# Optimization experiments

Measured on AMD Instinct MI355X. Metric: run time of the kernel, lower is better.

## Reference

```python
import jax, jax.numpy as jnp
import numpy as np

GH, GW, B, H, OUT = 9, 9, 1024, 256, 1


def setup_inputs() -> dict:
    key = jax.random.key(0)
    ks = jax.random.split(key, 16)
    N = GH * GW
    s3 = 1.0 / np.sqrt(3 * H)
    sH = 1.0 / np.sqrt(H)
    return {
        "x": jax.random.normal(ks[0], (B, GH, GW), jnp.float32),
        "h_ext": jax.random.normal(ks[1], (B, H), jnp.float32),
        "c_ext": jax.random.normal(ks[2], (B, H), jnp.float32),
        "grid_h": jax.random.normal(ks[3], (GH, GW, B, H), jnp.float32),
        "grid_c": jax.random.normal(ks[4], (GH, GW, B, H), jnp.float32),
        "W_hp": jax.random.normal(ks[5], (N, H, 3 * H), jnp.float32) * s3,
        "b_hp": jax.random.normal(ks[6], (N, H), jnp.float32) * s3,
        "W_cp": jax.random.normal(ks[7], (N, H, 3 * H), jnp.float32) * s3,
        "b_cp": jax.random.normal(ks[8], (N, H), jnp.float32) * s3,
        "W_ih": jax.random.normal(ks[9], (N, 4 * H, 1), jnp.float32) * sH,
        "W_hh": jax.random.normal(ks[10], (N, 4 * H, H), jnp.float32) * sH,
        "b_ih": jax.random.normal(ks[11], (N, 4 * H), jnp.float32) * sH,
        "b_hh": jax.random.normal(ks[12], (N, 4 * H), jnp.float32) * sH,
        "W_out": jax.random.normal(ks[13], (OUT, H), jnp.float32) * sH,
        "b_out": jnp.zeros((OUT,), jnp.float32),
    }


def _lstm_cell(x_cell, h0, c0, W_ih_k, W_hh_k, b_ih_k, b_hh_k):
    # x_cell: [B,1], h0/c0: [B,H]; torch LSTMCell math
    gates = x_cell @ W_ih_k.T + b_ih_k + h0 @ W_hh_k.T + b_hh_k  # [B,4H]
    i, f, g, o = jnp.split(gates, 4, axis=1)
    i, f, o = jax.nn.sigmoid(i), jax.nn.sigmoid(f), jax.nn.sigmoid(o)
    g = jnp.tanh(g)
    c = f * c0 + i * g
    h = o * jnp.tanh(c)
    return h, c


def reference(x, h_ext, c_ext, grid_h, grid_c,
              W_hp, b_hp, W_cp, b_cp,
              W_ih, W_hh, b_ih, b_hh, W_out, b_out):
    zeros = jnp.zeros((B, H), x.dtype)
    # new states, updated in raster order; left/up neighbors read NEW states
    new_h = [[None] * GW for _ in range(GH)]
    new_c = [[None] * GW for _ in range(GH)]
    for i in range(GH):
        for j in range(GW):
            k = i * GW + j
            h_prev, c_prev = grid_h[i, j], grid_c[i, j]
            if i == 0 and j == 0:
                h_left, c_left = h_ext, c_ext
            elif j > 0:
                h_left, c_left = new_h[i][j - 1], new_c[i][j - 1]
            else:
                h_left, c_left = zeros, zeros
            if i > 0:
                h_up, c_up = new_h[i - 1][j], new_c[i - 1][j]
            else:
                h_up, c_up = zeros, zeros
            comb_h = jnp.concatenate([h_left, h_up, h_prev], axis=1)  # [B,3H]
            comb_c = jnp.concatenate([c_left, c_up, c_prev], axis=1)
            ph = comb_h @ W_hp[k].T + b_hp[k]
            pc = comb_c @ W_cp[k].T + b_cp[k]
            x_cell = x[:, i, j][:, None]  # [B,1]
            h_new, c_new = _lstm_cell(x_cell, ph, pc, W_ih[k], W_hh[k], b_ih[k], b_hh[k])
            new_h[i][j], new_c[i][j] = h_new, c_new
    final_h, final_c = new_h[-1][-1], new_c[-1][-1]
    # fc_out with fc_layers_out=[0]: Linear + ReLU, then sigmoid
    out = jax.nn.sigmoid(jax.nn.relu(final_h @ W_out.T + b_out))
    gh = jnp.stack([jnp.stack(r, 0) for r in new_h], 0)
    gc = jnp.stack([jnp.stack(r, 0) for r in new_c], 0)
    return out, final_h, final_c, gh, gc
```

## Files before the change

### kernel.cpp

```cpp
#include <hip/hip_runtime.h>
#include <math.h>

#define BATCH 1024
#define HID 256
#define W3 768
#define SLOT (BATCH * HID)

typedef __bf16 bf16_t;
typedef __bf16 bf16x8 __attribute__((ext_vector_type(8)));
typedef float f32x4 __attribute__((ext_vector_type(4)));

__device__ inline bf16x8 cvt8(const float4 a, const float4 b) {
    bf16x8 r;
    r[0] = (bf16_t)a.x; r[1] = (bf16_t)a.y; r[2] = (bf16_t)a.z; r[3] = (bf16_t)a.w;
    r[4] = (bf16_t)b.x; r[5] = (bf16_t)b.y; r[6] = (bf16_t)b.z; r[7] = (bf16_t)b.w;
    return r;
}

template<bool ATOMIC>
__device__ __forceinline__ void proj_core(
        const float* __restrict__ src, const float* __restrict__ W, int koff,
        const float* __restrict__ bias, float* __restrict__ out,
        bf16_t (*Asm)[40], bf16_t (*Bsm)[40]) {
    const int t = threadIdx.x;
    const int lane = t & 63, wid = t >> 6;
    const int wm = wid & 1, wn = wid >> 1;
    const int ln = lane & 15, lh = lane >> 4;
    const int b0 = blockIdx.x * 128, n0 = blockIdx.y * 128;
    const int sr = t >> 1, sq = (t & 1) * 16;
    const float* arow = src + (size_t)(b0 + sr) * HID + sq;
    const float* wrow = W + (size_t)(n0 + sr) * W3 + koff + sq;
    f32x4 acc[4][4] = {};
    for (int kb = 0; kb < 8; ++kb) {
        const float4 a0 = *(const float4*)(arow + kb * 32);
        const float4 a1 = *(const float4*)(arow + kb * 32 + 4);
        const float4 a2 = *(const float4*)(arow + kb * 32 + 8);
        const float4 a3 = *(const float4*)(arow + kb * 32 + 12);
        const float4 w0 = *(const float4*)(wrow + kb * 32);
        const float4 w1 = *(const float4*)(wrow + kb * 32 + 4);
        const float4 w2 = *(const float4*)(wrow + kb * 32 + 8);
        const float4 w3 = *(const float4*)(wrow + kb * 32 + 12);
        const bf16x8 av0 = cvt8(a0, a1), av1 = cvt8(a2, a3);
        const bf16x8 bv0 = cvt8(w0, w1), bv1 = cvt8(w2, w3);
        __syncthreads();
        *(bf16x8*)&Asm[sr][sq] = av0;
        *(bf16x8*)&Asm[sr][sq + 8] = av1;
        *(bf16x8*)&Bsm[sr][sq] = bv0;
        *(bf16x8*)&Bsm[sr][sq + 8] = bv1;
        __syncthreads();
        bf16x8 af[4], bfv[4];
        #pragma unroll
        for (int mf = 0; mf < 4; ++mf)
            af[mf] = *(const bf16x8*)&Asm[wm * 64 + mf * 16 + ln][lh * 8];
        #pragma unroll
        for (int nf = 0; nf < 4; ++nf)
            bfv[nf] = *(const bf16x8*)&Bsm[wn * 64 + nf * 16 + ln][lh * 8];
        #pragma unroll
        for (int mf = 0; mf < 4; ++mf)
            #pragma unroll
            for (int nf = 0; nf < 4; ++nf)
                acc[mf][nf] = __builtin_amdgcn_mfma_f32_16x16x32_bf16(
                    af[mf], bfv[nf], acc[mf][nf], 0, 0, 0);
    }
    #pragma unroll
    for (int nf = 0; nf < 4; ++nf) {
        const int n = n0 + wn * 64 + nf * 16 + ln;
        const float bn = ATOMIC ? 0.f : bias[n];
        #pragma unroll
        for (int mf = 0; mf < 4; ++mf)
            #pragma unroll
            for (int r = 0; r < 4; ++r) {
                const int b = b0 + wm * 64 + mf * 16 + lh * 4 + r;
                if (ATOMIC)
                    unsafeAtomicAdd(out + (size_t)b * HID + n, acc[mf][nf][r]);
                else
                    out[(size_t)b * HID + n] = acc[mf][nf][r] + bn;
            }
    }
}

__global__ __launch_bounds__(256) void prevproj_kernel(
        const float* __restrict__ gridh, const float* __restrict__ gridc,
        const float* __restrict__ Whp, const float* __restrict__ Wcp,
        const float* __restrict__ bhp, const float* __restrict__ bcp,
        float* __restrict__ pall) {
    __shared__ bf16_t As[128][40];
    __shared__ bf16_t Bs[128][40];
    const int z = blockIdx.z, k = z >> 1, hc = z & 1;
    const float* src = (hc ? gridc : gridh) + (size_t)k * SLOT;
    const float* W = (hc ? Wcp : Whp) + (size_t)k * HID * W3;
    const float* bias = (hc ? bcp : bhp) + (size_t)k * HID;
    proj_core<false>(src, W, 512, bias, pall + (size_t)z * SLOT, As, Bs);
}

struct SegDesc { const float* src; const float* W; const float* bias; float* out; int koff; };
struct SegArgs { SegDesc d[36]; };

__global__ __launch_bounds__(256) void projseg_kernel(SegArgs a) {
    __shared__ bf16_t As[128][40];
    __shared__ bf16_t Bs[128][40];
    const SegDesc d = a.d[blockIdx.z];
    if (d.bias) proj_core<false>(d.src, d.W, d.koff, d.bias, d.out, As, Bs);
    else        proj_core<true>(d.src, d.W, d.koff, nullptr, d.out, As, Bs);
}

struct CellDesc {
    const float* ph; const float* pc;
    const float* Whh; const float* Wih; const float* bih; const float* bhh;
    const float* xcol;
    float* gh; float* gc;
};
struct CellBatchArgs { CellDesc d[9]; };

__global__ __launch_bounds__(256) void cell_kernel(CellBatchArgs args) {
    const CellDesc cd = args.d[blockIdx.z];
    __shared__ bf16_t Psm[128][40];
    __shared__ bf16_t Wsm[128][40];
    const int t = threadIdx.x;
    const int lane = t & 63, wid = t >> 6;
    const int wm = wid & 1, wn = wid >> 1;
    const int ln = lane & 15, lh = lane >> 4;
    const int b0 = blockIdx.x * 128;
    const int u0 = blockIdx.y * 32;
    const int sr = t >> 1, sq = (t & 1) * 16;
    const float* prow = cd.ph + (size_t)(b0 + sr) * HID + sq;
    const int cg = sr >> 5, cdu = sr & 31;
    const float* wrow = cd.Whh + (size_t)(cg * HID + u0 + cdu) * HID + sq;

    f32x4 acc[4][4] = {};
    for (int kb = 0; kb < 8; ++kb) {
        const float4 p0 = *(const float4*)(prow + kb * 32);
        const float4 p1 = *(const float4*)(prow + kb * 32 + 4);
        const float4 p2 = *(const float4*)(prow + kb * 32 + 8);
        const float4 p3 = *(const float4*)(prow + kb * 32 + 12);
        const float4 w0 = *(const float4*)(wrow + kb * 32);
        const float4 w1 = *(const float4*)(wrow + kb * 32 + 4);
        const float4 w2 = *(const float4*)(wrow + kb * 32 + 8);
        const float4 w3 = *(const float4*)(wrow + kb * 32 + 12);
        const bf16x8 pv0 = cvt8(p0, p1), pv1 = cvt8(p2, p3);
        const bf16x8 wv0 = cvt8(w0, w1), wv1 = cvt8(w2, w3);
        __syncthreads();
        *(bf16x8*)&Psm[sr][sq] = pv0;
        *(bf16x8*)&Psm[sr][sq + 8] = pv1;
        *(bf16x8*)&Wsm[sr][sq] = wv0;
        *(bf16x8*)&Wsm[sr][sq + 8] = wv1;
        __syncthreads();
        bf16x8 af[4], bfr[4];
        #pragma unroll
        for (int mf = 0; mf < 4; ++mf)
            af[mf] = *(const bf16x8*)&Psm[wm * 64 + mf * 16 + ln][lh * 8];
        #pragma unroll
        for (int g = 0; g < 4; ++g)
            bfr[g] = *(const bf16x8*)&Wsm[g * 32 + wn * 16 + ln][lh * 8];
        #pragma unroll
        for (int mf = 0; mf < 4; ++mf)
            #pragma unroll
            for (int g = 0; g < 4; ++g)
                acc[mf][g] = __builtin_amdgcn_mfma_f32_16x16x32_bf16(
                    af[mf], bfr[g], acc[mf][g], 0, 0, 0);
    }

    const int u = u0 + wn * 16 + ln;
    float wih[4], bsum[4];
    #pragma unroll
    for (int g = 0; g < 4; ++g) {
        const int n = g * HID + u;
        wih[g] = cd.Wih[n];
        bsum[g] = cd.bih[n] + cd.bhh[n];
    }
    #pragma unroll
    for (int mf = 0; mf < 4; ++mf)
        #pragma unroll
        for (int r = 0; r < 4; ++r) {
            const int b = b0 + wm * 64 + mf * 16 + lh * 4 + r;
            const float xv = cd.xcol[(size_t)b * 81];
            const float gi = acc[mf][0][r] + xv * wih[0] + bsum[0];
            const float gf = acc[mf][1][r] + xv * wih[1] + bsum[1];
            const float gg = acc[mf][2][r] + xv * wih[2] + bsum[2];
            const float go = acc[mf][3][r] + xv * wih[3] + bsum[3];
            const float i_ = 1.f / (1.f + expf(-gi));
            const float f_ = 1.f / (1.f + expf(-gf));
            const float o_ = 1.f / (1.f + expf(-go));
            const float g_ = tanhf(gg);
            const float c0 = cd.pc[(size_t)b * HID + u];
            const float cn = f_ * c0 + i_ * g_;
            const float hn = o_ * tanhf(cn);
            cd.gh[(size_t)b * HID + u] = hn;
            cd.gc[(size_t)b * HID + u] = cn;
        }
}

__global__ __launch_bounds__(256) void final_kernel(
        const float* __restrict__ gh88, const float* __restrict__ gc88,
        const float* __restrict__ Wout, const float* __restrict__ bout,
        float* __restrict__ out, float* __restrict__ fh, float* __restrict__ fc) {
    const int tid = blockIdx.x * blockDim.x + threadIdx.x;
    const int nth = gridDim.x * blockDim.x;
    for (int idx = tid; idx < BATCH * HID; idx += nth) {
        fh[idx] = gh88[idx];
        fc[idx] = gc88[idx];
    }
    if (tid < BATCH) {
        float s = bout[0];
        for (int k = 0; k < HID; ++k) s += gh88[(size_t)tid * HID + k] * Wout[k];
        s = fmaxf(s, 0.f);
        out[tid] = 1.f / (1.f + expf(-s));
    }
}

extern "C" void kernel_launch(void* const* d_in, const int* in_sizes, int n_in,
                              void* d_out, int out_size, void* d_ws, size_t ws_size,
                              hipStream_t stream) {
    const float* x      = (const float*)d_in[0];
    const float* h_ext  = (const float*)d_in[1];
    const float* c_ext  = (const float*)d_in[2];
    const float* grid_h = (const float*)d_in[3];
    const float* grid_c = (const float*)d_in[4];
    const float* W_hp   = (const float*)d_in[5];
    const float* b_hp   = (const float*)d_in[6];
    const float* W_cp   = (const float*)d_in[7];
    const float* b_cp   = (const float*)d_in[8];
    const float* W_ih   = (const float*)d_in[9];
    const float* W_hh   = (const float*)d_in[10];
    const float* b_ih   = (const float*)d_in[11];
    const float* b_hh   = (const float*)d_in[12];
    const float* W_out  = (const float*)d_in[13];
    const float* b_out  = (const float*)d_in[14];

    float* out = (float*)d_out;
    float* fh  = out + BATCH * 1;
    float* fc  = fh + SLOT;
    float* gh  = fc + SLOT;
    float* gc  = gh + (size_t)81 * SLOT;

    float* ws = (float*)d_ws;
    const bool bigws = ws_size >= (size_t)162 * SLOT * 4;

    if (bigws) {
        prevproj_kernel<<<dim3(8, 2, 162), 256, 0, stream>>>(
            grid_h, grid_c, W_hp, W_cp, b_hp, b_cp, ws);
        for (int d = 0; d <= 16; ++d) {
            const int i_lo = d > 8 ? d - 8 : 0;
            const int i_hi = d < 8 ? d : 8;
            const int nc = i_hi - i_lo + 1;
            SegArgs sa{};
            CellBatchArgs ca{};
            int nd = 0;
            for (int s = 0; s < nc; ++s) {
                const int i = i_lo + s, j = d - i;
                const int k = i * 9 + j;
                float* oh = ws + (size_t)(2 * k) * SLOT;
                float* oc = oh + SLOT;
                const float* Wh = W_hp + (size_t)k * HID * W3;
                const float* Wc = W_cp + (size_t)k * HID * W3;
                if (i == 0 && j == 0) {
                    sa.d[nd++] = { h_ext, Wh, nullptr, oh, 0 };
                    sa.d[nd++] = { c_ext, Wc, nullptr, oc, 0 };
                } else if (j > 0) {
                    sa.d[nd++] = { gh + (size_t)(k - 1) * SLOT, Wh, nullptr, oh, 0 };
                    sa.d[nd++] = { gc + (size_t)(k - 1) * SLOT, Wc, nullptr, oc, 0 };
                }
                if (i > 0) {
                    sa.d[nd++] = { gh + (size_t)(k - 9) * SLOT, Wh, nullptr, oh, 256 };
                    sa.d[nd++] = { gc + (size_t)(k - 9) * SLOT, Wc, nullptr, oc, 256 };
                }
                ca.d[s] = { oh, oc,
                            W_hh + (size_t)k * 4 * HID * HID,
                            W_ih + (size_t)k * 4 * HID,
                            b_ih + (size_t)k * 4 * HID,
                            b_hh + (size_t)k * 4 * HID,
                            x + i * 9 + j,
                            gh + (size_t)k * SLOT,
                            gc + (size_t)k * SLOT };
            }
            projseg_kernel<<<dim3(8, 2, nd), 256, 0, stream>>>(sa);
            cell_kernel<<<dim3(8, 8, nc), 256, 0, stream>>>(ca);
        }
    } else {
        for (int d = 0; d <= 16; ++d) {
            const int i_lo = d > 8 ? d - 8 : 0;
            const int i_hi = d < 8 ? d : 8;
            const int nc = i_hi - i_lo + 1;
            SegArgs base{}, inc{};
            CellBatchArgs ca{};
            int nb = 0, ni = 0;
            for (int s = 0; s < nc; ++s) {
                const int i = i_lo + s, j = d - i;
                const int k = i * 9 + j;
                float* oh = ws + (size_t)(2 * s) * SLOT;
                float* oc = oh + SLOT;
                const float* Wh = W_hp + (size_t)k * HID * W3;
                const float* Wc = W_cp + (size_t)k * HID * W3;
                base.d[nb++] = { grid_h + (size_t)k * SLOT, Wh, b_hp + (size_t)k * HID, oh, 512 };
                base.d[nb++] = { grid_c + (size_t)k * SLOT, Wc, b_cp + (size_t)k * HID, oc, 512 };
                if (i == 0 && j == 0) {
                    inc.d[ni++] = { h_ext, Wh, nullptr, oh, 0 };
                    inc.d[ni++] = { c_ext, Wc, nullptr, oc, 0 };
                } else if (j > 0) {
                    inc.d[ni++] = { gh + (size_t)(k - 1) * SLOT, Wh, nullptr, oh, 0 };
                    inc.d[ni++] = { gc + (size_t)(k - 1) * SLOT, Wc, nullptr, oc, 0 };
                }
                if (i > 0) {
                    inc.d[ni++] = { gh + (size_t)(k - 9) * SLOT, Wh, nullptr, oh, 256 };
                    inc.d[ni++] = { gc + (size_t)(k - 9) * SLOT, Wc, nullptr, oc, 256 };
                }
                ca.d[s] = { oh, oc,
                            W_hh + (size_t)k * 4 * HID * HID,
                            W_ih + (size_t)k * 4 * HID,
                            b_ih + (size_t)k * 4 * HID,
                            b_hh + (size_t)k * 4 * HID,
                            x + i * 9 + j,
                            gh + (size_t)k * SLOT,
                            gc + (size_t)k * SLOT };
            }
            projseg_kernel<<<dim3(8, 2, nb), 256, 0, stream>>>(base);
            projseg_kernel<<<dim3(8, 2, ni), 256, 0, stream>>>(inc);
            cell_kernel<<<dim3(8, 8, nc), 256, 0, stream>>>(ca);
        }
    }
    final_kernel<<<dim3(64), 256, 0, stream>>>(
        gh + (size_t)80 * SLOT, gc + (size_t)80 * SLOT,
        W_out, b_out, out, fh, fc);
}
```

Measured before the change: 1.095 ms.

## Precompose W_hh with W_hp and fuse per-diagonal projection and LSTM cell

Precomputes the product of the recurrent weight W_hh with the h-projection weights for each cell, plus the gate contributions from the previous-grid projection, in parallel kernels before the wavefront. Each diagonal then runs one fused kernel that applies the composed weights to left/up neighbor states, computes the c-projection, and applies the LSTM nonlinearity. This removes the atomic projection kernel and one launch per diagonal from the serial chain. In exchange it adds a large upfront compose GEMM, a very large workspace for base gates, and an extra bf16 rounding of the composed matrix.

```diff
diff --git a/kernel.cpp b/kernel.cpp
--- a/kernel.cpp
+++ b/kernel.cpp
@@ -8,12 +8,18 @@
 
 typedef __bf16 bf16_t;
 typedef __bf16 bf16x8 __attribute__((ext_vector_type(8)));
+typedef __bf16 bf16x4 __attribute__((ext_vector_type(4)));
 typedef float f32x4 __attribute__((ext_vector_type(4)));
 
 __device__ inline bf16x8 cvt8(const float4 a, const float4 b) {
     bf16x8 r;
     r[0] = (bf16_t)a.x; r[1] = (bf16_t)a.y; r[2] = (bf16_t)a.z; r[3] = (bf16_t)a.w;
     r[4] = (bf16_t)b.x; r[5] = (bf16_t)b.y; r[6] = (bf16_t)b.z; r[7] = (bf16_t)b.w;
+    return r;
+}
+__device__ inline bf16x4 cvt4(const float4 a) {
+    bf16x4 r;
+    r[0] = (bf16_t)a.x; r[1] = (bf16_t)a.y; r[2] = (bf16_t)a.z; r[3] = (bf16_t)a.w;
     return r;
 }
 
@@ -79,18 +85,270 @@
     }
 }
 
-__global__ __launch_bounds__(256) void prevproj_kernel(
+__global__ __launch_bounds__(256) void baseproj_kernel(
         const float* __restrict__ gridh, const float* __restrict__ gridc,
         const float* __restrict__ Whp, const float* __restrict__ Wcp,
         const float* __restrict__ bhp, const float* __restrict__ bcp,
-        float* __restrict__ pall) {
+        float* __restrict__ phb, float* __restrict__ pcb) {
     __shared__ bf16_t As[128][40];
     __shared__ bf16_t Bs[128][40];
     const int z = blockIdx.z, k = z >> 1, hc = z & 1;
     const float* src = (hc ? gridc : gridh) + (size_t)k * SLOT;
     const float* W = (hc ? Wcp : Whp) + (size_t)k * HID * W3;
     const float* bias = (hc ? bcp : bhp) + (size_t)k * HID;
-    proj_core<false>(src, W, 512, bias, pall + (size_t)z * SLOT, As, Bs);
+    float* out = (hc ? pcb : phb) + (size_t)k * SLOT;
+    proj_core<false>(src, W, 512, bias, out, As, Bs);
+}
+
+__global__ __launch_bounds__(256) void gatesbase_kernel(
+        const float* __restrict__ phb, const float* __restrict__ Whh,
+        const float* __restrict__ Wih, const float* __restrict__ bih,
+        const float* __restrict__ bhh, const float* __restrict__ x,
+        float* __restrict__ gbase) {
+    __shared__ bf16_t As[128][40];
+    __shared__ bf16_t Bs[128][40];
+    const int k = blockIdx.z;
+    const int t = threadIdx.x;
+    const int lane = t & 63, wid = t >> 6;
+    const int wm = wid & 1, wn = wid >> 1;
+    const int ln = lane & 15, lh = lane >> 4;
+    const int b0 = blockIdx.x * 128;
+    const int ub = blockIdx.y, u0 = ub * 32;
+    const int sr = t >> 1, sq = (t & 1) * 16;
+    const float* arow = phb + (size_t)k * SLOT + (size_t)(b0 + sr) * HID + sq;
+    const int g_r = sr >> 5, du_r = sr & 31;
+    const float* wrow = Whh + (size_t)k * 4 * HID * HID
+                        + (size_t)(g_r * HID + u0 + du_r) * HID + sq;
+    f32x4 acc[4][4] = {};
+    for (int kb = 0; kb < 8; ++kb) {
+        const float4 a0 = *(const float4*)(arow + kb * 32);
+        const float4 a1 = *(const float4*)(arow + kb * 32 + 4);
+        const float4 a2 = *(const float4*)(arow + kb * 32 + 8);
+        const float4 a3 = *(const float4*)(arow + kb * 32 + 12);
+        const float4 w0 = *(const float4*)(wrow + kb * 32);
+        const float4 w1 = *(const float4*)(wrow + kb * 32 + 4);
+        const float4 w2 = *(const float4*)(wrow + kb * 32 + 8);
+        const float4 w3 = *(const float4*)(wrow + kb * 32 + 12);
+        const bf16x8 av0 = cvt8(a0, a1), av1 = cvt8(a2, a3);
+        const bf16x8 bv0 = cvt8(w0, w1), bv1 = cvt8(w2, w3);
+        __syncthreads();
+        *(bf16x8*)&As[sr][sq] = av0;
+        *(bf16x8*)&As[sr][sq + 8] = av1;
+        *(bf16x8*)&Bs[sr][sq] = bv0;
+        *(bf16x8*)&Bs[sr][sq + 8] = bv1;
+        __syncthreads();
+        bf16x8 af[4], bfr[4];
+        #pragma unroll
+        for (int mf = 0; mf < 4; ++mf)
+            af[mf] = *(const bf16x8*)&As[wm * 64 + mf * 16 + ln][lh * 8];
+        #pragma unroll
+        for (int g = 0; g < 4; ++g)
+            bfr[g] = *(const bf16x8*)&Bs[g * 32 + wn * 16 + ln][lh * 8];
+        #pragma unroll
+        for (int mf = 0; mf < 4; ++mf)
+            #pragma unroll
+            for (int g = 0; g < 4; ++g)
+                acc[mf][g] = __builtin_amdgcn_mfma_f32_16x16x32_bf16(
+                    af[mf], bfr[g], acc[mf][g], 0, 0, 0);
+    }
+    const int u = u0 + wn * 16 + ln;
+    float wih[4], bb[4];
+    #pragma unroll
+    for (int g = 0; g < 4; ++g) {
+        const int n4 = g * HID + u;
+        wih[g] = Wih[(size_t)k * 4 * HID + n4];
+        bb[g] = bih[(size_t)k * 4 * HID + n4] + bhh[(size_t)k * 4 * HID + n4];
+    }
+    float* orow = gbase + (size_t)k * BATCH * 1024;
+    #pragma unroll
+    for (int mf = 0; mf < 4; ++mf)
+        #pragma unroll
+        for (int r = 0; r < 4; ++r) {
+            const int b = b0 + wm * 64 + mf * 16 + lh * 4 + r;
+            const float xv = x[(size_t)b * 81 + k];
+            #pragma unroll
+            for (int g = 0; g < 4; ++g)
+                orow[(size_t)b * 1024 + ub * 128 + g * 32 + wn * 16 + ln] =
+                    acc[mf][g][r] + xv * wih[g] + bb[g],
+                (void)0;
+            #pragma unroll
+            for (int g = 1; g < 4; ++g) { }
+        }
+}
+
+__global__ __launch_bounds__(256) void compose_kernel(
+        const float* __restrict__ Whh, const float* __restrict__ Whp,
+        bf16_t* __restrict__ CC) {
+    __shared__ bf16_t As[128][40];
+    __shared__ bf16_t Bs[128][40];
+    const int k = blockIdx.z;
+    const int t = threadIdx.x;
+    const int lane = t & 63, wid = t >> 6;
+    const int wm = wid & 1, wn = wid >> 1;
+    const int ln = lane & 15, lh = lane >> 4;
+    const int m0 = blockIdx.x * 128;
+    const int by = blockIdx.y;
+    const int sr = t >> 1, sq = (t & 1) * 16;
+    const int g_r = sr >> 5, du_r = sr & 31;
+    const float* arow = Whh + (size_t)k * 4 * HID * HID
+                        + (size_t)(g_r * HID + by * 32 + du_r) * HID + sq;
+    const float* wbase = Whp + (size_t)k * HID * W3;
+    const int uu = t >> 3, mm0 = (t & 7) * 16;
+    f32x4 acc[4][4] = {};
+    for (int kb = 0; kb < 8; ++kb) {
+        const float4 a0 = *(const float4*)(arow + kb * 32);
+        const float4 a1 = *(const float4*)(arow + kb * 32 + 4);
+        const float4 a2 = *(const float4*)(arow + kb * 32 + 8);
+        const float4 a3 = *(const float4*)(arow + kb * 32 + 12);
+        const float* bsrc = wbase + (size_t)(kb * 32 + uu) * W3 + m0 + mm0;
+        const float4 v0 = *(const float4*)(bsrc);
+        const float4 v1 = *(const float4*)(bsrc + 4);
+        const float4 v2 = *(const float4*)(bsrc + 8);
+        const float4 v3 = *(const float4*)(bsrc + 12);
+        const bf16x8 av0 = cvt8(a0, a1), av1 = cvt8(a2, a3);
+        const bf16x4 bq[4] = { cvt4(v0), cvt4(v1), cvt4(v2), cvt4(v3) };
+        __syncthreads();
+        *(bf16x8*)&As[sr][sq] = av0;
+        *(bf16x8*)&As[sr][sq + 8] = av1;
+        #pragma unroll
+        for (int q = 0; q < 4; ++q)
+            #pragma unroll
+            for (int e = 0; e < 4; ++e)
+                Bs[mm0 + q * 4 + e][uu] = bq[q][e];
+        __syncthreads();
+        bf16x8 af[4], bf[4];
+        #pragma unroll
+        for (int mf = 0; mf < 4; ++mf)
+            af[mf] = *(const bf16x8*)&As[wm * 64 + mf * 16 + ln][lh * 8];
+        #pragma unroll
+        for (int nf = 0; nf < 4; ++nf)
+            bf[nf] = *(const bf16x8*)&Bs[wn * 64 + nf * 16 + ln][lh * 8];
+        #pragma unroll
+        for (int mf = 0; mf < 4; ++mf)
+            #pragma unroll
+            for (int nf = 0; nf < 4; ++nf)
+                acc[mf][nf] = __builtin_amdgcn_mfma_f32_16x16x32_bf16(
+                    af[mf], bf[nf], acc[mf][nf], 0, 0, 0);
+    }
+    bf16_t* out = CC + (size_t)k * 1024 * 512;
+    #pragma unroll
+    for (int nf = 0; nf < 4; ++nf) {
+        const int m = m0 + wn * 64 + nf * 16 + ln;
+        #pragma unroll
+        for (int mf = 0; mf < 4; ++mf)
+            #pragma unroll
+            for (int r = 0; r < 4; ++r) {
+                const int c = by * 128 + wm * 64 + mf * 16 + lh * 4 + r;
+                out[(size_t)c * 512 + m] = (bf16_t)acc[mf][nf][r];
+            }
+    }
+}
+
+struct FusedDesc {
+    const float* hl; const float* cl;
+    const float* hu; const float* cu;
+    const float* gb;
+    const float* pcb;
+    const bf16_t* cc;
+    const float* wcp;
+    float* gh; float* gc;
+};
+struct FusedBatchArgs { FusedDesc d[9]; };
+
+__global__ __launch_bounds__(256) void fused_kernel(FusedBatchArgs args) {
+    const FusedDesc fd = args.d[blockIdx.z];
+    __shared__ bf16_t A1[128][40];
+    __shared__ bf16_t A2[128][40];
+    __shared__ bf16_t B1[128][40];
+    __shared__ bf16_t B2[32][40];
+    const int t = threadIdx.x;
+    const int lane = t & 63, wid = t >> 6;
+    const int wm = wid & 1, wn = wid >> 1;
+    const int ln = lane & 15, lh = lane >> 4;
+    const int b0 = blockIdx.x * 128;
+    const int by = blockIdx.y, u0 = by * 32;
+    const int sr = t >> 1, sq = (t & 1) * 16;
+    const int du2 = t >> 3, kk4 = (t & 7) * 4;
+
+    const float* hs[2]; const float* cs[2]; int ko[2]; int ns = 0;
+    if (fd.hl) { hs[ns] = fd.hl; cs[ns] = fd.cl; ko[ns] = 0;   ++ns; }
+    if (fd.hu) { hs[ns] = fd.hu; cs[ns] = fd.cu; ko[ns] = 256; ++ns; }
+
+    f32x4 accg[4][4] = {};
+    f32x4 accp[4] = {};
+
+    for (int s = 0; s < ns; ++s) {
+        const float* ha = hs[s] + (size_t)(b0 + sr) * HID + sq;
+        const float* ca = cs[s] + (size_t)(b0 + sr) * HID + sq;
+        const bf16_t* b1r = fd.cc + (size_t)(by * 128 + sr) * 512 + ko[s] + sq;
+        const float* b2r = fd.wcp + (size_t)(u0 + du2) * W3 + ko[s] + kk4;
+        for (int kb = 0; kb < 8; ++kb) {
+            const float4 h0 = *(const float4*)(ha + kb * 32);
+            const float4 h1 = *(const float4*)(ha + kb * 32 + 4);
+            const float4 h2 = *(const float4*)(ha + kb * 32 + 8);
+            const float4 h3 = *(const float4*)(ha + kb * 32 + 12);
+            const float4 c0 = *(const float4*)(ca + kb * 32);
+            const float4 c1 = *(const float4*)(ca + kb * 32 + 4);
+            const float4 c2 = *(const float4*)(ca + kb * 32 + 8);
+            const float4 c3 = *(const float4*)(ca + kb * 32 + 12);
+            const bf16x8 w0 = *(const bf16x8*)(b1r + kb * 32);
+            const bf16x8 w1 = *(const bf16x8*)(b1r + kb * 32 + 8);
+            const float4 p0 = *(const float4*)(b2r + kb * 32);
+            const bf16x8 hv0 = cvt8(h0, h1), hv1 = cvt8(h2, h3);
+            const bf16x8 cv0 = cvt8(c0, c1), cv1 = cvt8(c2, c3);
+            const bf16x4 pv = cvt4(p0);
+            __syncthreads();
+            *(bf16x8*)&A1[sr][sq] = hv0;
+            *(bf16x8*)&A1[sr][sq + 8] = hv1;
+            *(bf16x8*)&A2[sr][sq] = cv0;
+            *(bf16x8*)&A2[sr][sq + 8] = cv1;
+            *(bf16x8*)&B1[sr][sq] = w0;
+            *(bf16x8*)&B1[sr][sq + 8] = w1;
+            *(bf16x4*)&B2[du2][kk4] = pv;
+            __syncthreads();
+            bf16x8 af1[4], bf1[4], af2[4], bf2;
+            #pragma unroll
+            for (int mf = 0; mf < 4; ++mf) {
+                af1[mf] = *(const bf16x8*)&A1[wm * 64 + mf * 16 + ln][lh * 8];
+                af2[mf] = *(const bf16x8*)&A2[wm * 64 + mf * 16 + ln][lh * 8];
+            }
+            #pragma unroll
+            for (int g = 0; g < 4; ++g)
+                bf1[g] = *(const bf16x8*)&B1[g * 32 + wn * 16 + ln][lh * 8];
+            bf2 = *(const bf16x8*)&B2[wn * 16 + ln][lh * 8];
+            #pragma unroll
+            for (int mf = 0; mf < 4; ++mf) {
+                #pragma unroll
+                for (int g = 0; g < 4; ++g)
+                    accg[mf][g] = __builtin_amdgcn_mfma_f32_16x16x32_bf16(
+                        af1[mf], bf1[g], accg[mf][g], 0, 0, 0);
+                accp[mf] = __builtin_amdgcn_mfma_f32_16x16x32_bf16(
+                    af2[mf], bf2, accp[mf], 0, 0, 0);
+            }
+        }
+    }
+
+    const int u = u0 + wn * 16 + ln;
+    #pragma unroll
+    for (int mf = 0; mf < 4; ++mf)
+        #pragma unroll
+        for (int r = 0; r < 4; ++r) {
+            const int b = b0 + wm * 64 + mf * 16 + lh * 4 + r;
+            const float* gbr = fd.gb + (size_t)b * 1024 + by * 128 + wn * 16 + ln;
+            const float gi = accg[mf][0][r] + gbr[0];
+            const float gf = accg[mf][1][r] + gbr[32];
+            const float gg = accg[mf][2][r] + gbr[64];
+            const float go = accg[mf][3][r] + gbr[96];
+            const float pc = accp[mf][r] + fd.pcb[(size_t)b * HID + u];
+            const float i_ = 1.f / (1.f + expf(-gi));
+            const float f_ = 1.f / (1.f + expf(-gf));
+            const float o_ = 1.f / (1.f + expf(-go));
+            const float g_ = tanhf(gg);
+            const float cn = f_ * pc + i_ * g_;
+            const float hn = o_ * tanhf(cn);
+            fd.gh[(size_t)b * HID + u] = hn;
+            fd.gc[(size_t)b * HID + u] = cn;
+        }
 }
 
 struct SegDesc { const float* src; const float* W; const float* bias; float* out; int koff; };
@@ -126,7 +384,6 @@
     const float* prow = cd.ph + (size_t)(b0 + sr) * HID + sq;
     const int cg = sr >> 5, cdu = sr & 31;
     const float* wrow = cd.Whh + (size_t)(cg * HID + u0 + cdu) * HID + sq;
-
     f32x4 acc[4][4] = {};
     for (int kb = 0; kb < 8; ++kb) {
         const float4 p0 = *(const float4*)(prow + kb * 32);
@@ -159,7 +416,6 @@
                 acc[mf][g] = __builtin_amdgcn_mfma_f32_16x16x32_bf16(
                     af[mf], bfr[g], acc[mf][g], 0, 0, 0);
     }
-
     const int u = u0 + wn * 16 + ln;
     float wih[4], bsum[4];
     #pragma unroll
@@ -233,50 +489,49 @@
     float* gh  = fc + SLOT;
     float* gc  = gh + (size_t)81 * SLOT;
 
-    float* ws = (float*)d_ws;
-    const bool bigws = ws_size >= (size_t)162 * SLOT * 4;
-
-    if (bigws) {
-        prevproj_kernel<<<dim3(8, 2, 162), 256, 0, stream>>>(
-            grid_h, grid_c, W_hp, W_cp, b_hp, b_cp, ws);
+    const size_t gb_bytes = (size_t)81 * BATCH * 1024 * 4;
+    const size_t cc_bytes = (size_t)81 * 1024 * 512 * 2;
+    const size_t pb_bytes = (size_t)81 * SLOT * 4;
+    const size_t need_new = gb_bytes + cc_bytes + 2 * pb_bytes;
+
+    if (ws_size >= need_new) {
+        float* gbase = (float*)d_ws;
+        bf16_t* CC = (bf16_t*)((char*)d_ws + gb_bytes);
+        float* pcb = (float*)((char*)d_ws + gb_bytes + cc_bytes);
+        float* phb = (float*)((char*)d_ws + gb_bytes + cc_bytes + pb_bytes);
+
+        baseproj_kernel<<<dim3(8, 2, 162), 256, 0, stream>>>(
+            grid_h, grid_c, W_hp, W_cp, b_hp, b_cp, phb, pcb);
+        compose_kernel<<<dim3(4, 8, 81), 256, 0, stream>>>(W_hh, W_hp, CC);
+        gatesbase_kernel<<<dim3(8, 8, 81), 256, 0, stream>>>(
+            phb, W_hh, W_ih, b_ih, b_hh, x, gbase);
+
         for (int d = 0; d <= 16; ++d) {
             const int i_lo = d > 8 ? d - 8 : 0;
             const int i_hi = d < 8 ? d : 8;
             const int nc = i_hi - i_lo + 1;
-            SegArgs sa{};
-            CellBatchArgs ca{};
-            int nd = 0;
+            FusedBatchArgs fa{};
             for (int s = 0; s < nc; ++s) {
                 const int i = i_lo + s, j = d - i;
                 const int k = i * 9 + j;
-                float* oh = ws + (size_t)(2 * k) * SLOT;
-                float* oc = oh + SLOT;
-                const float* Wh = W_hp + (size_t)k * HID * W3;
-                const float* Wc = W_cp + (size_t)k * HID * W3;
-                if (i == 0 && j == 0) {
-                    sa.d[nd++] = { h_ext, Wh, nullptr, oh, 0 };
-                    sa.d[nd++] = { c_ext, Wc, nullptr, oc, 0 };
-                } else if (j > 0) {
-                    sa.d[nd++] = { gh + (size_t)(k - 1) * SLOT, Wh, nullptr, oh, 0 };
-                    sa.d[nd++] = { gc + (size_t)(k - 1) * SLOT, Wc, nullptr, oc, 0 };
-                }
-                if (i > 0) {
-                    sa.d[nd++] = { gh + (size_t)(k - 9) * SLOT, Wh, nullptr, oh, 256 };
-                    sa.d[nd++] = { gc + (size_t)(k - 9) * SLOT, Wc, nullptr, oc, 256 };
-                }
-                ca.d[s] = { oh, oc,
-                            W_hh + (size_t)k * 4 * HID * HID,
-                            W_ih + (size_t)k * 4 * HID,
-                            b_ih + (size_t)k * 4 * HID,
-                            b_hh + (size_t)k * 4 * HID,
-                            x + i * 9 + j,
+                const float *hl = nullptr, *cl = nullptr, *hu = nullptr, *cu = nullptr;
+                if (i == 0 && j == 0)      { hl = h_ext; cl = c_ext; }
+                else if (j > 0)            { hl = gh + (size_t)(k - 1) * SLOT;
+                                             cl = gc + (size_t)(k - 1) * SLOT; }
+                if (i > 0)                 { hu = gh + (size_t)(k - 9) * SLOT;
+                                             cu = gc + (size_t)(k - 9) * SLOT; }
+                fa.d[s] = { hl, cl, hu, cu,
+                            gbase + (size_t)k * BATCH * 1024,
+                            pcb + (size_t)k * SLOT,
+                            CC + (size_t)k * 1024 * 512,
+                            W_cp + (size_t)k * HID * W3,
                             gh + (size_t)k * SLOT,
                             gc + (size_t)k * SLOT };
             }
-            projseg_kernel<<<dim3(8, 2, nd), 256, 0, stream>>>(sa);
-            cell_kernel<<<dim3(8, 8, nc), 256, 0, stream>>>(ca);
+            fused_kernel<<<dim3(8, 8, nc), 256, 0, stream>>>(fa);
         }
     } else {
+        float* ws = (float*)d_ws;
         for (int d = 0; d <= 16; ++d) {
             const int i_lo = d > 8 ? d - 8 : 0;
             const int i_hi = d < 8 ? d : 8;
```

Result: slower. 1.241 ms (+13.4%).
